# Kernel tuning notes

Hardware: AMD Instinct MI355X
Metric: run time of the kernel (lower is better)

The kernel has to match this reference:

```python
import jax, jax.numpy as jnp
import numpy as np

N = 4096      # sequence length (tokens)
D = 256       # model_dim
H = 4         # num_heads
DH = D // H   # dim_per_head = 64
TOPK = 30     # dot_attention default
SCALE = float((DH // H) ** -0.5)  # torch: (key.size(-1)//num_heads)**-0.5 = 16**-0.5 = 0.25
LN_EPS = 1e-5


def setup_inputs() -> dict:
    key = jax.random.key(0)
    ks = jax.random.split(key, 11)
    s = 0.02
    return {
        "key_in":   jax.random.normal(ks[0], (N, D), jnp.float32),
        "value_in": jax.random.normal(ks[1], (N, D), jnp.float32),
        "query_in": jax.random.normal(ks[2], (N, D), jnp.float32),
        "Wq": jax.random.normal(ks[3], (D, D), jnp.float32) * s,
        "bq": jax.random.normal(ks[4], (D,), jnp.float32) * s,
        "Wk": jax.random.normal(ks[5], (D, D), jnp.float32) * s,
        "bk": jax.random.normal(ks[6], (D,), jnp.float32) * s,
        "Wv": jax.random.normal(ks[7], (D, D), jnp.float32) * s,
        "bv": jax.random.normal(ks[8], (D,), jnp.float32) * s,
        "Wo": jax.random.normal(ks[9], (D, D), jnp.float32) * s,
        "bo": jax.random.normal(ks[10], (D,), jnp.float32) * s,
        "ln_g": jnp.ones((D,), jnp.float32),
        "ln_b": jnp.zeros((D,), jnp.float32),
    }


def reference(key_in, value_in, query_in, Wq, bq, Wk, bk, Wv, bv, Wo, bo, ln_g, ln_b):
    # Projections (nn.Linear: x @ W.T + b)
    q = query_in @ Wq.T + bq            # (N, D)
    k = key_in @ Wk.T + bk
    v = value_in @ Wv.T + bv
    # view(N, H, DH).transpose(0,1) -> (H, N, DH)
    qh = q.reshape(N, H, DH).transpose(1, 0, 2)
    kh = k.reshape(N, H, DH).transpose(1, 0, 2)
    vh = v.reshape(N, H, DH).transpose(1, 0, 2)

    scores = jnp.einsum('hnd,hmd->hnm', qh, kh) * SCALE   # (H, N, N)

    # top-k mask via scatter (faithful to torch.topk + scatter_)
    idx = jax.lax.top_k(scores, TOPK)[1]                  # (H, N, TOPK)
    mask = jnp.zeros_like(scores).at[
        jnp.arange(H)[:, None, None],
        jnp.arange(N)[None, :, None],
        idx].set(1.0)
    masked = jnp.where(mask > 0, scores, -jnp.inf)
    attn = jax.nn.softmax(masked, axis=-1)                # (H, N, N); dropout p=0 -> identity

    ctx = jnp.einsum('hnm,hmd->hnd', attn, vh)            # (H, N, DH)
    ctx = ctx.transpose(1, 0, 2).reshape(N, D)

    out = ctx @ Wo.T + bo
    resid = query_in + out                                # residual is pre-projection query
    mu = resid.mean(axis=-1, keepdims=True)
    var = resid.var(axis=-1, keepdims=True)               # biased var, like torch LayerNorm
    out = (resid - mu) / jnp.sqrt(var + LN_EPS) * ln_g + ln_b
    return out, attn
```

## Files before the change

### kernel.cpp

```cpp
#include <hip/hip_runtime.h>
#include <stdint.h>

#define N_TOK 4096
#define DIM   256
#define NH    4
#define DH    64
#define TOPK  30
#define CANDN 40
#define ATT_SCALE 0.25f
#define LN_EPS 1e-5f

typedef __attribute__((ext_vector_type(8))) short bf16x8;
typedef __attribute__((ext_vector_type(4))) float f32x4;

static __device__ __forceinline__ ushort f2bf(float f) {
    uint x = __float_as_uint(f);
    return (ushort)((x + 0x7FFFu + ((x >> 16) & 1u)) >> 16);
}
static __device__ __forceinline__ bf16x8 load_frag(const ushort* p) {
    union { int4 i; bf16x8 f; } u;
    u.i = *reinterpret_cast<const int4*>(p);
    return u.f;
}
static __device__ __forceinline__ uint s16key(uint u) {
    return (u & 0x8000u) ? (u ^ 0xFFFFu) : (u | 0x8000u);
}

#define BK 32
__global__ __launch_bounds__(256) void qk_gemm_f32(
    const float* __restrict__ query_in, const float* __restrict__ key_in,
    const float* __restrict__ Wq, const float* __restrict__ bq,
    const float* __restrict__ Wk, const float* __restrict__ bk,
    float* __restrict__ qf, float* __restrict__ kf,
    ushort* __restrict__ qb, ushort* __restrict__ kb)
{
    const int j0g = blockIdx.x * 64;
    const int sel = j0g >> 8;
    const int j0  = j0g & 255;
    const float* A    = sel ? key_in : query_in;
    const float* W    = sel ? Wk : Wq;
    const float* bias = sel ? bk : bq;
    float*  outF = sel ? kf : qf;
    ushort* outB = sel ? kb : qb;

    __shared__ float As[BK][64 + 4];
    __shared__ float Ws[BK][64 + 4];
    const int tid = threadIdx.x;
    const int tx = tid & 15;
    const int ty = tid >> 4;
    const int i0 = blockIdx.y * 64;

    float acc[4][4];
#pragma unroll
    for (int r = 0; r < 4; r++)
#pragma unroll
        for (int c = 0; c < 4; c++) acc[r][c] = 0.f;

    for (int k0 = 0; k0 < DIM; k0 += BK) {
#pragma unroll
        for (int u = 0; u < 2; u++) {
            const int f = u * 256 + tid;
            const int r = f >> 3;
            const int c = (f & 7) * 4;
            float4 va = *reinterpret_cast<const float4*>(A + (size_t)(i0 + r) * DIM + k0 + c);
            As[c + 0][r] = va.x; As[c + 1][r] = va.y;
            As[c + 2][r] = va.z; As[c + 3][r] = va.w;
            float4 vw = *reinterpret_cast<const float4*>(W + (size_t)(j0 + r) * DIM + k0 + c);
            Ws[c + 0][r] = vw.x; Ws[c + 1][r] = vw.y;
            Ws[c + 2][r] = vw.z; Ws[c + 3][r] = vw.w;
        }
        __syncthreads();
#pragma unroll
        for (int kk = 0; kk < BK; kk++) {
            const float4 a4 = *reinterpret_cast<const float4*>(&As[kk][ty * 4]);
            const float4 b4 = *reinterpret_cast<const float4*>(&Ws[kk][tx * 4]);
            const float ar[4] = {a4.x, a4.y, a4.z, a4.w};
            const float br[4] = {b4.x, b4.y, b4.z, b4.w};
#pragma unroll
            for (int r = 0; r < 4; r++)
#pragma unroll
                for (int c = 0; c < 4; c++) acc[r][c] += ar[r] * br[c];
        }
        __syncthreads();
    }

#pragma unroll
    for (int r = 0; r < 4; r++) {
        const int gi = i0 + ty * 4 + r;
#pragma unroll
        for (int c = 0; c < 4; c++) {
            const int gj = j0 + tx * 4 + c;
            float v = acc[r][c] + bias[gj];
            outF[(size_t)gi * DIM + gj] = v;
            outB[(size_t)gi * DIM + gj] = f2bf(v);
        }
    }
}

__global__ __launch_bounds__(256) void cast_kernel(
    const float* __restrict__ value_in, const float* __restrict__ Wv,
    const float* __restrict__ Wo, ushort* __restrict__ value_b,
    ushort* __restrict__ Wv_b, ushort* __restrict__ Wo_b)
{
    const int id4 = blockIdx.x * 256 + threadIdx.x;
    const int NV = 1048576 / 4, NW = 65536 / 4;
    const float* src; ushort* dst; int off;
    if (id4 < NV)            { src = value_in; dst = value_b; off = id4; }
    else if (id4 < NV + NW)  { src = Wv; dst = Wv_b; off = id4 - NV; }
    else                     { src = Wo; dst = Wo_b; off = id4 - NV - NW; }
    float4 v = reinterpret_cast<const float4*>(src)[off];
    ushort4 o = {f2bf(v.x), f2bf(v.y), f2bf(v.z), f2bf(v.w)};
    reinterpret_cast<ushort4*>(dst)[off] = o;
}

__global__ __launch_bounds__(256) void mfma_gemm(
    const ushort* __restrict__ A, const ushort* __restrict__ B,
    const float* __restrict__ bias, const float* __restrict__ addX,
    float* __restrict__ outF)
{
    const int lane = threadIdx.x & 63;
    const int wv   = threadIdx.x >> 6;
    const int i0   = blockIdx.y * 64 + wv * 16;
    const int j0   = blockIdx.x * 64;
    const int r = lane & 15, q = lane >> 4;

    f32x4 acc[4];
#pragma unroll
    for (int b = 0; b < 4; b++) acc[b] = (f32x4){0.f, 0.f, 0.f, 0.f};

#pragma unroll
    for (int ks = 0; ks < 8; ks++) {
        const int kk = ks * 32 + q * 8;
        bf16x8 af = load_frag(A + (size_t)(i0 + r) * DIM + kk);
        bf16x8 bfr[4];
#pragma unroll
        for (int jt = 0; jt < 4; jt++)
            bfr[jt] = load_frag(B + (size_t)(j0 + jt * 16 + r) * DIM + kk);
#pragma unroll
        for (int jt = 0; jt < 4; jt++)
            acc[jt] = __builtin_amdgcn_mfma_f32_16x16x32_bf16(af, bfr[jt], acc[jt], 0, 0, 0);
    }

#pragma unroll
    for (int jt = 0; jt < 4; jt++) {
        const int gj = j0 + jt * 16 + r;
        const float bv = bias[gj];
#pragma unroll
        for (int rg = 0; rg < 4; rg++) {
            const int gi = i0 + q * 4 + rg;
            float v = acc[jt][rg] + bv;
            if (addX) v += addX[(size_t)gi * DIM + gj];
            outF[(size_t)gi * DIM + gj] = v;
        }
    }
}

__global__ __launch_bounds__(256) void scores_kernel(
    const ushort* __restrict__ qb, const ushort* __restrict__ kb,
    ushort* __restrict__ sb)
{
    const int lane = threadIdx.x & 63;
    const int wv   = threadIdx.x >> 6;
    const int h    = blockIdx.z;
    const int i0   = blockIdx.y * 128 + wv * 32;
    const int j0   = blockIdx.x * 128;
    const int r = lane & 15, q = lane >> 4;
    const int koff = h * DH;

    f32x4 acc[2][8];
#pragma unroll
    for (int a = 0; a < 2; a++)
#pragma unroll
        for (int b = 0; b < 8; b++) acc[a][b] = (f32x4){0.f, 0.f, 0.f, 0.f};

#pragma unroll
    for (int ks = 0; ks < 2; ks++) {
        const int kk = koff + ks * 32 + q * 8;
        bf16x8 af[2], bfr[8];
#pragma unroll
        for (int mt = 0; mt < 2; mt++)
            af[mt] = load_frag(qb + (size_t)(i0 + mt * 16 + r) * DIM + kk);
#pragma unroll
        for (int jt = 0; jt < 8; jt++)
            bfr[jt] = load_frag(kb + (size_t)(j0 + jt * 16 + r) * DIM + kk);
#pragma unroll
        for (int mt = 0; mt < 2; mt++)
#pragma unroll
            for (int jt = 0; jt < 8; jt++)
                acc[mt][jt] = __builtin_amdgcn_mfma_f32_16x16x32_bf16(
                    af[mt], bfr[jt], acc[mt][jt], 0, 0, 0);
    }

#pragma unroll
    for (int mt = 0; mt < 2; mt++)
#pragma unroll
        for (int rg = 0; rg < 4; rg++) {
            const int gi = i0 + mt * 16 + q * 4 + rg;
            ushort* row = sb + ((size_t)(h * N_TOK + gi)) * N_TOK;
#pragma unroll
            for (int jt = 0; jt < 8; jt++)
                row[j0 + jt * 16 + r] = (ushort)s16key(f2bf(acc[mt][jt][rg]));
        }
}

__global__ __launch_bounds__(256) void select_kernel(
    const ushort* __restrict__ sb, const float* __restrict__ qf,
    const float* __restrict__ kf, const float* __restrict__ vf,
    float* __restrict__ pval, int* __restrict__ pidx,
    ushort* __restrict__ ctxb)
{
    const int lane = threadIdx.x & 63;
    const int wv   = threadIdx.x >> 6;
    const int row  = blockIdx.x * 4 + wv;
    const int h    = row >> 12;
    const int i    = row & (N_TOK - 1);
    const ushort* srow = sb + (size_t)row * N_TOK;

    __shared__ uint  hist[4][256];
    __shared__ uint  cand[4][64];
    __shared__ uint  ccnt[4];
    __shared__ float pw[4][TOPK];
    __shared__ int   jw[4][TOPK];
    __shared__ __align__(16) float qsh[4][DH];

    qsh[wv][lane] = qf[(size_t)i * DIM + h * DH + lane];
    if (lane == 0) ccnt[wv] = 0;
#pragma unroll
    for (int b = 0; b < 4; b++) hist[wv][b * 64 + lane] = 0u;

    uint kw[32];
    const int4* srow4 = reinterpret_cast<const int4*>(srow);
#pragma unroll
    for (int t = 0; t < 8; t++) {
        int4 c = srow4[t * 64 + lane];
        kw[t * 4 + 0] = (uint)c.x; kw[t * 4 + 1] = (uint)c.y;
        kw[t * 4 + 2] = (uint)c.z; kw[t * 4 + 3] = (uint)c.w;
    }

    uint mx = 0;
#pragma unroll
    for (int w = 0; w < 32; w++) {
        uint lo16 = kw[w] & 0xFFFFu, hi16 = kw[w] >> 16;
        mx = max(mx, max(lo16, hi16));
    }
#pragma unroll
    for (int off = 32; off; off >>= 1)
        mx = max(mx, (uint)__shfl_xor((int)mx, off));

    __syncthreads();

#pragma unroll
    for (int w = 0; w < 32; w++) {
        uint d0 = mx - (kw[w] & 0xFFFFu);
        uint d1 = mx - (kw[w] >> 16);
        if (d0 < 255u) atomicAdd(&hist[wv][d0], 1u);
        if (d1 < 255u) atomicAdd(&hist[wv][d1], 1u);
    }
    __syncthreads();

    const uint c0 = hist[wv][lane * 4 + 0];
    const uint c1 = hist[wv][lane * 4 + 1];
    const uint c2 = hist[wv][lane * 4 + 2];
    const uint c3 = hist[wv][lane * 4 + 3];
    const uint seg = c0 + c1 + c2 + c3;
    uint scan = seg;
#pragma unroll
    for (int d = 1; d < 64; d <<= 1) {
        uint y = (uint)__shfl_up((int)scan, d);
        if (lane >= d) scan += y;
    }
    const uint excl = scan - seg;
    const bool crossing = (excl < CANDN) && (scan >= CANDN);
    unsigned long long bal = __ballot(crossing);

    int t = 256;
    if (bal != 0ull) {
        const int srcLane = __ffsll(bal) - 1;
        int tloc = lane * 4;
        if (crossing) {
            uint cum = excl + c0;
            if (cum < CANDN) { tloc++; cum += c1;
                if (cum < CANDN) { tloc++; cum += c2;
                    if (cum < CANDN) { tloc++; } } }
        }
        t = __shfl(tloc, srcLane);
    }

    uint T;
    if (t <= 254) {
        T = mx - (uint)t;
    } else {
        uint lo = 0;
#pragma unroll
        for (int b = 15; b >= 0; b--) {
            uint trial = lo | (1u << b);
            int c = 0;
#pragma unroll
            for (int w = 0; w < 32; w++) {
                c += ((kw[w] & 0xFFFFu) >= trial) ? 1 : 0;
                c += ((kw[w] >> 16)     >= trial) ? 1 : 0;
            }
#pragma unroll
            for (int off = 32; off; off >>= 1) c += __shfl_xor(c, off);
            if (c >= CANDN) lo = trial;
        }
        T = lo;
    }

#pragma unroll
    for (int w = 0; w < 32; w++) {
        const uint lo16 = kw[w] & 0xFFFFu, hi16 = kw[w] >> 16;
        const int jbase = (w >> 2) * 512 + lane * 8 + (w & 3) * 2;
        if (lo16 >= T) {
            uint pos = atomicAdd(&ccnt[wv], 1u);
            if (pos < 64u) cand[wv][pos] = (uint)jbase;
        }
        if (hi16 >= T) {
            uint pos = atomicAdd(&ccnt[wv], 1u);
            if (pos < 64u) cand[wv][pos] = (uint)(jbase + 1);
        }
    }
    __syncthreads();
    const int m = (int)min(ccnt[wv], 64u);

    unsigned long long ukey = 0ull;
    if (lane < m) {
        const int j = (int)cand[wv][lane];
        const float4* kr = reinterpret_cast<const float4*>(kf + (size_t)j * DIM + h * DH);
        const float4* qr = reinterpret_cast<const float4*>(qsh[wv]);
        float s = 0.f;
#pragma unroll
        for (int d = 0; d < 16; d++) {
            float4 a = qr[d], bb = kr[d];
            s += a.x * bb.x; s += a.y * bb.y; s += a.z * bb.z; s += a.w * bb.w;
        }
        uint bits = __float_as_uint(s);
        uint s32 = (bits & 0x80000000u) ? ~bits : (bits | 0x80000000u);
        ukey = ((unsigned long long)s32 << 12) | (unsigned long long)(4095 - j);
    }

#pragma unroll
    for (int k = 2; k <= 64; k <<= 1) {
#pragma unroll
        for (int jj = k >> 1; jj > 0; jj >>= 1) {
            unsigned long long o = __shfl_xor(ukey, jj);
            bool keepMax = ((lane & jj) != 0) ^ ((lane & k) != 0);
            ukey = keepMax ? (ukey > o ? ukey : o) : (ukey < o ? ukey : o);
        }
    }

    const int rank = 63 - lane;
    const int jsel = 4095 - (int)(ukey & 0xFFFull);
    uint s32b = (uint)(ukey >> 12);
    uint fb = (s32b & 0x80000000u) ? (s32b ^ 0x80000000u) : ~s32b;
    const float sc = __uint_as_float(fb);
    const float stop = __shfl(sc, 63);

    float e = (rank < TOPK) ? __expf((sc - stop) * ATT_SCALE) : 0.f;
    float esum = e;
#pragma unroll
    for (int off = 32; off; off >>= 1) esum += __shfl_xor(esum, off);
    const float p = e / esum;

    if (rank < TOPK) {
        pw[wv][rank] = p; jw[wv][rank] = jsel;
        pval[(size_t)row * 32 + rank] = p;
        pidx[(size_t)row * 32 + rank] = jsel;
    }
    __syncthreads();

    float a = 0.f;
#pragma unroll
    for (int c = 0; c < TOPK; c++)
        a += pw[wv][c] * vf[(size_t)jw[wv][c] * DIM + h * DH + lane];
    ctxb[(size_t)i * DIM + h * DH + lane] = f2bf(a);
}

__global__ __launch_bounds__(256) void attn_write(
    const float* __restrict__ pval, const int* __restrict__ pidx,
    float* __restrict__ attnF)
{
    __shared__ __align__(16) float rb[4][N_TOK];
    const int tid = threadIdx.x;
    const int r0 = blockIdx.x * 4;

    float4* rb4 = reinterpret_cast<float4*>(&rb[0][0]);
    const float4 z = {0.f, 0.f, 0.f, 0.f};
#pragma unroll
    for (int t = 0; t < 16; t++) rb4[t * 256 + tid] = z;
    __syncthreads();
    if (tid < 4 * TOPK) {
        const int w = tid / TOPK, c = tid % TOPK;
        rb[w][pidx[(size_t)(r0 + w) * 32 + c]] = pval[(size_t)(r0 + w) * 32 + c];
    }
    __syncthreads();
#pragma unroll
    for (int w = 0; w < 4; w++) {
        float4* grow = reinterpret_cast<float4*>(attnF + (size_t)(r0 + w) * N_TOK);
#pragma unroll
        for (int t = 0; t < 4; t++)
            grow[t * 256 + tid] = rb4[w * 1024 + t * 256 + tid];
    }
}

__global__ __launch_bounds__(64) void ln_kernel(
    float* __restrict__ resb, const float* __restrict__ g,
    const float* __restrict__ b)
{
    const int i = blockIdx.x, lane = threadIdx.x;
    float4* rowp = reinterpret_cast<float4*>(resb + (size_t)i * DIM);
    float4 x = rowp[lane];
    float s  = x.x + x.y + x.z + x.w;
    float sq = x.x * x.x + x.y * x.y + x.z * x.z + x.w * x.w;
#pragma unroll
    for (int off = 32; off; off >>= 1) {
        s  += __shfl_xor(s, off);
        sq += __shfl_xor(sq, off);
    }
    const float mu  = s * (1.f / DIM);
    const float var = sq * (1.f / DIM) - mu * mu;
    const float rstd = rsqrtf(var + LN_EPS);
    const int col = lane * 4;
    float4 o;
    o.x = (x.x - mu) * rstd * g[col + 0] + b[col + 0];
    o.y = (x.y - mu) * rstd * g[col + 1] + b[col + 1];
    o.z = (x.z - mu) * rstd * g[col + 2] + b[col + 2];
    o.w = (x.w - mu) * rstd * g[col + 3] + b[col + 3];
    rowp[lane] = o;
}

extern "C" void kernel_launch(void* const* d_in, const int* in_sizes, int n_in,
                              void* d_out, int out_size, void* d_ws, size_t ws_size,
                              hipStream_t stream)
{
    const float* key_in   = (const float*)d_in[0];
    const float* value_in = (const float*)d_in[1];
    const float* query_in = (const float*)d_in[2];
    const float* Wq = (const float*)d_in[3];
    const float* bq = (const float*)d_in[4];
    const float* Wk = (const float*)d_in[5];
    const float* bk = (const float*)d_in[6];
    const float* Wv = (const float*)d_in[7];
    const float* bv = (const float*)d_in[8];
    const float* Wo = (const float*)d_in[9];
    const float* bo = (const float*)d_in[10];
    const float* ln_g = (const float*)d_in[11];
    const float* ln_b = (const float*)d_in[12];

    float* outF  = (float*)d_out;
    float* attnF = outF + (size_t)N_TOK * DIM;

    const size_t SC = 33554432;
    ushort* sb   = (ushort*)attnF;
    float*  qf   = attnF + SC;
    float*  kf   = attnF + SC + 1048576;
    float*  vf   = attnF + SC + 2097152;
    ushort* qb   = (ushort*)(attnF + SC + 3145728);
    ushort* kb   = (ushort*)(attnF + SC + 3670016);
    ushort* ctxb = (ushort*)(attnF + SC + 4194304);

    float*  pval    = (float*)d_ws;
    int*    pidx    = (int*)d_ws + 524288;
    ushort* value_b = (ushort*)((char*)d_ws + (4u << 20));
    ushort* Wv_b    = (ushort*)((char*)d_ws + (6u << 20));
    ushort* Wo_b    = (ushort*)((char*)d_ws + (6u << 20) + 131072);

    cast_kernel<<<dim3((1048576 + 65536 + 65536) / 4 / 256), 256, 0, stream>>>(
        value_in, Wv, Wo, value_b, Wv_b, Wo_b);
    qk_gemm_f32<<<dim3(8, 64), 256, 0, stream>>>(
        query_in, key_in, Wq, bq, Wk, bk, qf, kf, qb, kb);
    mfma_gemm<<<dim3(4, 64), 256, 0, stream>>>(value_b, Wv_b, bv, nullptr, vf);

    scores_kernel<<<dim3(32, 32, NH), 256, 0, stream>>>(qb, kb, sb);
    select_kernel<<<dim3(N_TOK * NH / 4), 256, 0, stream>>>(
        sb, qf, kf, vf, pval, pidx, ctxb);

    mfma_gemm<<<dim3(4, 64), 256, 0, stream>>>(ctxb, Wo_b, bo, query_in, outF);
    ln_kernel<<<N_TOK, 64, 0, stream>>>(outF, ln_g, ln_b);

    attn_write<<<N_TOK * NH / 4, 256, 0, stream>>>(pval, pidx, attnF);
}
```

Baseline: 440.5 us.

## Fuse attention-matrix write into select kernel and stage score stores via LDS

When the workspace is large enough, the score keys move into the workspace, so select_kernel can zero its attention row and scatter the top-k probabilities directly into the output. This drops the separate attn_write pass and the pval/pidx round-trip. The scores kernel now stages each wave's tile in shared memory and writes 16-byte coalesced rows instead of scattered 2-byte stores. Several block-wide barriers are removed because each wave only touches its own shared slices. Ordering between the zero-fill and the scatter relies on an explicit s_waitcnt, and the path needs a workspace of more than 128MB.

```diff
diff --git a/kernel.cpp b/kernel.cpp
--- a/kernel.cpp
+++ b/kernel.cpp
@@ -167,6 +167,8 @@
     const int r = lane & 15, q = lane >> 4;
     const int koff = h * DH;
 
+    __shared__ ushort st[4][32][136];
+
     f32x4 acc[2][8];
 #pragma unroll
     for (int a = 0; a < 2; a++)
@@ -194,20 +196,27 @@
 #pragma unroll
     for (int mt = 0; mt < 2; mt++)
 #pragma unroll
-        for (int rg = 0; rg < 4; rg++) {
-            const int gi = i0 + mt * 16 + q * 4 + rg;
-            ushort* row = sb + ((size_t)(h * N_TOK + gi)) * N_TOK;
-#pragma unroll
-            for (int jt = 0; jt < 8; jt++)
-                row[j0 + jt * 16 + r] = (ushort)s16key(f2bf(acc[mt][jt][rg]));
-        }
+        for (int jt = 0; jt < 8; jt++)
+#pragma unroll
+            for (int rg = 0; rg < 4; rg++)
+                st[wv][mt * 16 + q * 4 + rg][jt * 16 + r] =
+                    (ushort)s16key(f2bf(acc[mt][jt][rg]));
+
+    const int rr = lane >> 4, seg = lane & 15;
+#pragma unroll
+    for (int it = 0; it < 8; it++) {
+        const int rowl = it * 4 + rr;
+        const int gi = i0 + rowl;
+        int4 vdat = *reinterpret_cast<const int4*>(&st[wv][rowl][seg * 8]);
+        *reinterpret_cast<int4*>(sb + ((size_t)(h * N_TOK + gi)) * N_TOK + j0 + seg * 8) = vdat;
+    }
 }
 
 __global__ __launch_bounds__(256) void select_kernel(
     const ushort* __restrict__ sb, const float* __restrict__ qf,
     const float* __restrict__ kf, const float* __restrict__ vf,
     float* __restrict__ pval, int* __restrict__ pidx,
-    ushort* __restrict__ ctxb)
+    ushort* __restrict__ ctxb, float* __restrict__ attnRow)
 {
     const int lane = threadIdx.x & 63;
     const int wv   = threadIdx.x >> 6;
@@ -247,8 +256,6 @@
     for (int off = 32; off; off >>= 1)
         mx = max(mx, (uint)__shfl_xor((int)mx, off));
 
-    __syncthreads();
-
 #pragma unroll
     for (int w = 0; w < 32; w++) {
         uint d0 = mx - (kw[w] & 0xFFFFu);
@@ -256,7 +263,6 @@
         if (d0 < 255u) atomicAdd(&hist[wv][d0], 1u);
         if (d1 < 255u) atomicAdd(&hist[wv][d1], 1u);
     }
-    __syncthreads();
 
     const uint c0 = hist[wv][lane * 4 + 0];
     const uint c1 = hist[wv][lane * 4 + 1];
@@ -307,6 +313,13 @@
         T = lo;
     }
 
+    if (attnRow) {
+        float4* rowg = reinterpret_cast<float4*>(attnRow + (size_t)row * N_TOK);
+        const float4 z = {0.f, 0.f, 0.f, 0.f};
+#pragma unroll
+        for (int tt = 0; tt < 16; tt++) rowg[tt * 64 + lane] = z;
+    }
+
 #pragma unroll
     for (int w = 0; w < 32; w++) {
         const uint lo16 = kw[w] & 0xFFFFu, hi16 = kw[w] >> 16;
@@ -320,7 +333,6 @@
             if (pos < 64u) cand[wv][pos] = (uint)(jbase + 1);
         }
     }
-    __syncthreads();
     const int m = (int)min(ccnt[wv], 64u);
 
     unsigned long long ukey = 0ull;
@@ -364,16 +376,23 @@
 
     if (rank < TOPK) {
         pw[wv][rank] = p; jw[wv][rank] = jsel;
-        pval[(size_t)row * 32 + rank] = p;
-        pidx[(size_t)row * 32 + rank] = jsel;
-    }
-    __syncthreads();
+        if (pval) {
+            pval[(size_t)row * 32 + rank] = p;
+            pidx[(size_t)row * 32 + rank] = jsel;
+        }
+    }
 
     float a = 0.f;
 #pragma unroll
     for (int c = 0; c < TOPK; c++)
         a += pw[wv][c] * vf[(size_t)jw[wv][c] * DIM + h * DH + lane];
     ctxb[(size_t)i * DIM + h * DH + lane] = f2bf(a);
+
+    if (attnRow) {
+        asm volatile("s_waitcnt vmcnt(0)" ::: "memory");
+        if (rank < TOPK)
+            attnRow[(size_t)row * N_TOK + jsel] = p;
+    }
 }
 
 __global__ __launch_bounds__(256) void attn_write(
@@ -450,33 +469,63 @@
     float* outF  = (float*)d_out;
     float* attnF = outF + (size_t)N_TOK * DIM;
 
-    const size_t SC = 33554432;
-    ushort* sb   = (ushort*)attnF;
-    float*  qf   = attnF + SC;
-    float*  kf   = attnF + SC + 1048576;
-    float*  vf   = attnF + SC + 2097152;
-    ushort* qb   = (ushort*)(attnF + SC + 3145728);
-    ushort* kb   = (ushort*)(attnF + SC + 3670016);
-    ushort* ctxb = (ushort*)(attnF + SC + 4194304);
-
-    float*  pval    = (float*)d_ws;
-    int*    pidx    = (int*)d_ws + 524288;
-    ushort* value_b = (ushort*)((char*)d_ws + (4u << 20));
-    ushort* Wv_b    = (ushort*)((char*)d_ws + (6u << 20));
-    ushort* Wo_b    = (ushort*)((char*)d_ws + (6u << 20) + 131072);
-
-    cast_kernel<<<dim3((1048576 + 65536 + 65536) / 4 / 256), 256, 0, stream>>>(
-        value_in, Wv, Wo, value_b, Wv_b, Wo_b);
-    qk_gemm_f32<<<dim3(8, 64), 256, 0, stream>>>(
-        query_in, key_in, Wq, bq, Wk, bk, qf, kf, qb, kb);
-    mfma_gemm<<<dim3(4, 64), 256, 0, stream>>>(value_b, Wv_b, bv, nullptr, vf);
-
-    scores_kernel<<<dim3(32, 32, NH), 256, 0, stream>>>(qb, kb, sb);
-    select_kernel<<<dim3(N_TOK * NH / 4), 256, 0, stream>>>(
-        sb, qf, kf, vf, pval, pidx, ctxb);
-
-    mfma_gemm<<<dim3(4, 64), 256, 0, stream>>>(ctxb, Wo_b, bo, query_in, outF);
-    ln_kernel<<<N_TOK, 64, 0, stream>>>(outF, ln_g, ln_b);
-
-    attn_write<<<N_TOK * NH / 4, 256, 0, stream>>>(pval, pidx, attnF);
-}
+    const size_t KEYB = (size_t)NH * N_TOK * N_TOK * 2;
+    const size_t NEED = KEYB + (21u << 20);
+
+    if (ws_size >= NEED) {
+        char* ws = (char*)d_ws;
+        ushort* sb      = (ushort*)ws;
+        float*  qf      = (float*)(ws + KEYB);
+        float*  kf      = (float*)(ws + KEYB + (4u  << 20));
+        float*  vf      = (float*)(ws + KEYB + (8u  << 20));
+        ushort* qb      = (ushort*)(ws + KEYB + (12u << 20));
+        ushort* kb      = (ushort*)(ws + KEYB + (14u << 20));
+        ushort* ctxb    = (ushort*)(ws + KEYB + (16u << 20));
+        ushort* value_b = (ushort*)(ws + KEYB + (18u << 20));
+        ushort* Wv_b    = (ushort*)(ws + KEYB + (20u << 20));
+        ushort* Wo_b    = (ushort*)(ws + KEYB + (20u << 20) + 131072);
+
+        cast_kernel<<<dim3((1048576 + 65536 + 65536) / 4 / 256), 256, 0, stream>>>(
+            value_in, Wv, Wo, value_b, Wv_b, Wo_b);
+        qk_gemm_f32<<<dim3(8, 64), 256, 0, stream>>>(
+            query_in, key_in, Wq, bq, Wk, bk, qf, kf, qb, kb);
+        mfma_gemm<<<dim3(4, 64), 256, 0, stream>>>(value_b, Wv_b, bv, nullptr, vf);
+
+        scores_kernel<<<dim3(32, 32, NH), 256, 0, stream>>>(qb, kb, sb);
+        select_kernel<<<dim3(N_TOK * NH / 4), 256, 0, stream>>>(
+            sb, qf, kf, vf, nullptr, nullptr, ctxb, attnF);
+
+        mfma_gemm<<<dim3(4, 64), 256, 0, stream>>>(ctxb, Wo_b, bo, query_in, outF);
+        ln_kernel<<<N_TOK, 64, 0, stream>>>(outF, ln_g, ln_b);
+    } else {
+        const size_t SC = 33554432;
+        ushort* sb   = (ushort*)attnF;
+        float*  qf   = attnF + SC;
+        float*  kf   = attnF + SC + 1048576;
+        float*  vf   = attnF + SC + 2097152;
+        ushort* qb   = (ushort*)(attnF + SC + 3145728);
+        ushort* kb   = (ushort*)(attnF + SC + 3670016);
+        ushort* ctxb = (ushort*)(attnF + SC + 4194304);
+
+        float*  pval    = (float*)d_ws;
+        int*    pidx    = (int*)d_ws + 524288;
+        ushort* value_b = (ushort*)((char*)d_ws + (4u << 20));
+        ushort* Wv_b    = (ushort*)((char*)d_ws + (6u << 20));
+        ushort* Wo_b    = (ushort*)((char*)d_ws + (6u << 20) + 131072);
+
+        cast_kernel<<<dim3((1048576 + 65536 + 65536) / 4 / 256), 256, 0, stream>>>(
+            value_in, Wv, Wo, value_b, Wv_b, Wo_b);
+        qk_gemm_f32<<<dim3(8, 64), 256, 0, stream>>>(
+            query_in, key_in, Wq, bq, Wk, bk, qf, kf, qb, kb);
+        mfma_gemm<<<dim3(4, 64), 256, 0, stream>>>(value_b, Wv_b, bv, nullptr, vf);
+
+        scores_kernel<<<dim3(32, 32, NH), 256, 0, stream>>>(qb, kb, sb);
+        select_kernel<<<dim3(N_TOK * NH / 4), 256, 0, stream>>>(
+            sb, qf, kf, vf, pval, pidx, ctxb, nullptr);
+
+        mfma_gemm<<<dim3(4, 64), 256, 0, stream>>>(ctxb, Wo_b, bo, query_in, outF);
+        ln_kernel<<<N_TOK, 64, 0, stream>>>(outF, ln_g, ln_b);
+
+        attn_write<<<N_TOK * NH / 4, 256, 0, stream>>>(pval, pidx, attnF);
+    }
+}
```

After: 471.3 us. 1.07x slower.

## Store attention scores as 8-bit fixed-point keys for top-k candidate selection

Applied to the files above, without the earlier changes.

The scores kernel now quantises each score to an 8-bit key (floor(s*32)+128, clamped), stages it in shared memory and writes coalesced 16-byte rows. This halves the scratch score matrix traffic between the scores and select kernels. The select kernel builds a histogram with a fixed floor instead of a per-row max, gathers up to 192 candidates and ranks them in multiple bitonic rounds. A full fp32 recompute fallback handles rows with too many candidates. Intermediate buffers move into the workspace. The coarse quantisation risks more candidates per row and extra exact-dot work, plus fallback cost on outlier rows.

```diff
diff --git a/kernel.cpp b/kernel.cpp
--- a/kernel.cpp
+++ b/kernel.cpp
@@ -6,12 +6,15 @@
 #define NH    4
 #define DH    64
 #define TOPK  30
-#define CANDN 40
+#define CANDN 56
+#define CANDCAP 192
+#define FLOORK8 173u
 #define ATT_SCALE 0.25f
 #define LN_EPS 1e-5f
 
 typedef __attribute__((ext_vector_type(8))) short bf16x8;
 typedef __attribute__((ext_vector_type(4))) float f32x4;
+typedef unsigned long long u64;
 
 static __device__ __forceinline__ ushort f2bf(float f) {
     uint x = __float_as_uint(f);
@@ -25,6 +28,12 @@
 static __device__ __forceinline__ uint s16key(uint u) {
     return (u & 0x8000u) ? (u ^ 0xFFFFu) : (u | 0x8000u);
 }
+static __device__ __forceinline__ uint f2k8(float s) {
+    int v = (int)floorf(s * 32.0f) + 128;
+    return (uint)min(max(v, 0), 255);
+}
+static __device__ __forceinline__ u64 u64max(u64 a, u64 b) { return a > b ? a : b; }
+static __device__ __forceinline__ u64 u64min(u64 a, u64 b) { return a < b ? a : b; }
 
 #define BK 32
 __global__ __launch_bounds__(256) void qk_gemm_f32(
@@ -103,7 +112,7 @@
     ushort* __restrict__ Wv_b, ushort* __restrict__ Wo_b)
 {
     const int id4 = blockIdx.x * 256 + threadIdx.x;
-    const int NV = 1048576 / 4, NW = 65536 / 4;
+    const int NV = 262144, NW = 16384;
     const float* src; ushort* dst; int off;
     if (id4 < NV)            { src = value_in; dst = value_b; off = id4; }
     else if (id4 < NV + NW)  { src = Wv; dst = Wv_b; off = id4 - NV; }
@@ -157,7 +166,7 @@
 
 __global__ __launch_bounds__(256) void scores_kernel(
     const ushort* __restrict__ qb, const ushort* __restrict__ kb,
-    ushort* __restrict__ sb)
+    uchar* __restrict__ sb)
 {
     const int lane = threadIdx.x & 63;
     const int wv   = threadIdx.x >> 6;
@@ -167,6 +176,8 @@
     const int r = lane & 15, q = lane >> 4;
     const int koff = h * DH;
 
+    __shared__ uchar st[4][32][144];
+
     f32x4 acc[2][8];
 #pragma unroll
     for (int a = 0; a < 2; a++)
@@ -194,17 +205,24 @@
 #pragma unroll
     for (int mt = 0; mt < 2; mt++)
 #pragma unroll
-        for (int rg = 0; rg < 4; rg++) {
-            const int gi = i0 + mt * 16 + q * 4 + rg;
-            ushort* row = sb + ((size_t)(h * N_TOK + gi)) * N_TOK;
-#pragma unroll
-            for (int jt = 0; jt < 8; jt++)
-                row[j0 + jt * 16 + r] = (ushort)s16key(f2bf(acc[mt][jt][rg]));
-        }
+        for (int jt = 0; jt < 8; jt++)
+#pragma unroll
+            for (int rg = 0; rg < 4; rg++)
+                st[wv][mt * 16 + q * 4 + rg][jt * 16 + r] =
+                    (uchar)f2k8(acc[mt][jt][rg]);
+
+    const int rr = lane >> 3, seg = lane & 7;
+#pragma unroll
+    for (int it = 0; it < 4; it++) {
+        const int rowl = it * 8 + rr;
+        const int gi = i0 + rowl;
+        int4 vdat = *reinterpret_cast<const int4*>(&st[wv][rowl][seg * 16]);
+        *reinterpret_cast<int4*>(sb + ((size_t)(h * N_TOK + gi)) * N_TOK + j0 + seg * 16) = vdat;
+    }
 }
 
 __global__ __launch_bounds__(256) void select_kernel(
-    const ushort* __restrict__ sb, const float* __restrict__ qf,
+    const uchar* __restrict__ sb, const float* __restrict__ qf,
     const float* __restrict__ kf, const float* __restrict__ vf,
     float* __restrict__ pval, int* __restrict__ pidx,
     ushort* __restrict__ ctxb)
@@ -214,13 +232,13 @@
     const int row  = blockIdx.x * 4 + wv;
     const int h    = row >> 12;
     const int i    = row & (N_TOK - 1);
-    const ushort* srow = sb + (size_t)row * N_TOK;
-
-    __shared__ uint  hist[4][256];
-    __shared__ uint  cand[4][64];
-    __shared__ uint  ccnt[4];
-    __shared__ float pw[4][TOPK];
-    __shared__ int   jw[4][TOPK];
+    const uchar* srow = sb + (size_t)row * N_TOK;
+
+    __shared__ uint   hist[4][256];
+    __shared__ ushort cand[4][CANDCAP];
+    __shared__ uint   ccnt[4];
+    __shared__ float  pw[4][TOPK];
+    __shared__ int    jw[4][TOPK];
     __shared__ __align__(16) float qsh[4][DH];
 
     qsh[wv][lane] = qf[(size_t)i * DIM + h * DH + lane];
@@ -228,35 +246,24 @@
 #pragma unroll
     for (int b = 0; b < 4; b++) hist[wv][b * 64 + lane] = 0u;
 
-    uint kw[32];
+    uint kw[16];
     const int4* srow4 = reinterpret_cast<const int4*>(srow);
 #pragma unroll
-    for (int t = 0; t < 8; t++) {
+    for (int t = 0; t < 4; t++) {
         int4 c = srow4[t * 64 + lane];
         kw[t * 4 + 0] = (uint)c.x; kw[t * 4 + 1] = (uint)c.y;
         kw[t * 4 + 2] = (uint)c.z; kw[t * 4 + 3] = (uint)c.w;
     }
 
-    uint mx = 0;
-#pragma unroll
-    for (int w = 0; w < 32; w++) {
-        uint lo16 = kw[w] & 0xFFFFu, hi16 = kw[w] >> 16;
-        mx = max(mx, max(lo16, hi16));
-    }
-#pragma unroll
-    for (int off = 32; off; off >>= 1)
-        mx = max(mx, (uint)__shfl_xor((int)mx, off));
-
-    __syncthreads();
-
-#pragma unroll
-    for (int w = 0; w < 32; w++) {
-        uint d0 = mx - (kw[w] & 0xFFFFu);
-        uint d1 = mx - (kw[w] >> 16);
-        if (d0 < 255u) atomicAdd(&hist[wv][d0], 1u);
-        if (d1 < 255u) atomicAdd(&hist[wv][d1], 1u);
-    }
-    __syncthreads();
+#pragma unroll
+    for (int w = 0; w < 16; w++) {
+        const uint x = kw[w];
+#pragma unroll
+        for (int b = 0; b < 4; b++) {
+            const uint k8 = (x >> (8 * b)) & 255u;
+            if (k8 >= FLOORK8) atomicAdd(&hist[wv][255u - k8], 1u);
+        }
+    }
 
     const uint c0 = hist[wv][lane * 4 + 0];
     const uint c1 = hist[wv][lane * 4 + 1];
@@ -273,7 +280,7 @@
     const bool crossing = (excl < CANDN) && (scan >= CANDN);
     unsigned long long bal = __ballot(crossing);
 
-    int t = 256;
+    uint Tk;
     if (bal != 0ull) {
         const int srcLane = __ffsll(bal) - 1;
         int tloc = lane * 4;
@@ -283,13 +290,56 @@
                 if (cum < CANDN) { tloc++; cum += c2;
                     if (cum < CANDN) { tloc++; } } }
         }
-        t = __shfl(tloc, srcLane);
-    }
-
-    uint T;
-    if (t <= 254) {
-        T = mx - (uint)t;
+        const int t = __shfl(tloc, srcLane);
+        Tk = 255u - (uint)t;
     } else {
+        uint lo = 0;
+#pragma unroll
+        for (int b = 7; b >= 0; b--) {
+            uint trial = lo | (1u << b);
+            int c = 0;
+#pragma unroll
+            for (int w = 0; w < 16; w++)
+#pragma unroll
+                for (int bb = 0; bb < 4; bb++)
+                    c += (((kw[w] >> (8 * bb)) & 255u) >= trial) ? 1 : 0;
+#pragma unroll
+            for (int off = 32; off; off >>= 1) c += __shfl_xor(c, off);
+            if (c >= CANDN) lo = trial;
+        }
+        Tk = lo;
+    }
+
+#pragma unroll
+    for (int w = 0; w < 16; w++) {
+        const uint x = kw[w];
+        const int jbase = (w >> 2) * 1024 + lane * 16 + (w & 3) * 4;
+#pragma unroll
+        for (int b = 0; b < 4; b++) {
+            if (((x >> (8 * b)) & 255u) >= Tk) {
+                uint pos = atomicAdd(&ccnt[wv], 1u);
+                if (pos < CANDCAP) cand[wv][pos] = (ushort)(jbase + b);
+            }
+        }
+    }
+
+    uint cnt = ccnt[wv];
+    if (cnt > CANDCAP) {
+        uint kwf[32];
+        const float4* qr = reinterpret_cast<const float4*>(qsh[wv]);
+        for (int tt = 0; tt < 64; tt++) {
+            const int j = tt * 64 + lane;
+            const float4* kr = reinterpret_cast<const float4*>(kf + (size_t)j * DIM + h * DH);
+            float s = 0.f;
+#pragma unroll
+            for (int d = 0; d < 16; d++) {
+                float4 a = qr[d], bb = kr[d];
+                s += a.x * bb.x; s += a.y * bb.y; s += a.z * bb.z; s += a.w * bb.w;
+            }
+            const uint key = s16key(f2bf(s));
+            if (tt & 1) kwf[tt >> 1] |= key << 16;
+            else        kwf[tt >> 1] = key;
+        }
         uint lo = 0;
 #pragma unroll
         for (int b = 15; b >= 0; b--) {
@@ -297,61 +347,68 @@
             int c = 0;
 #pragma unroll
             for (int w = 0; w < 32; w++) {
-                c += ((kw[w] & 0xFFFFu) >= trial) ? 1 : 0;
-                c += ((kw[w] >> 16)     >= trial) ? 1 : 0;
+                c += ((kwf[w] & 0xFFFFu) >= trial) ? 1 : 0;
+                c += ((kwf[w] >> 16)     >= trial) ? 1 : 0;
             }
 #pragma unroll
             for (int off = 32; off; off >>= 1) c += __shfl_xor(c, off);
-            if (c >= CANDN) lo = trial;
-        }
-        T = lo;
-    }
-
-#pragma unroll
-    for (int w = 0; w < 32; w++) {
-        const uint lo16 = kw[w] & 0xFFFFu, hi16 = kw[w] >> 16;
-        const int jbase = (w >> 2) * 512 + lane * 8 + (w & 3) * 2;
-        if (lo16 >= T) {
-            uint pos = atomicAdd(&ccnt[wv], 1u);
-            if (pos < 64u) cand[wv][pos] = (uint)jbase;
-        }
-        if (hi16 >= T) {
-            uint pos = atomicAdd(&ccnt[wv], 1u);
-            if (pos < 64u) cand[wv][pos] = (uint)(jbase + 1);
-        }
-    }
-    __syncthreads();
-    const int m = (int)min(ccnt[wv], 64u);
-
-    unsigned long long ukey = 0ull;
-    if (lane < m) {
-        const int j = (int)cand[wv][lane];
-        const float4* kr = reinterpret_cast<const float4*>(kf + (size_t)j * DIM + h * DH);
-        const float4* qr = reinterpret_cast<const float4*>(qsh[wv]);
-        float s = 0.f;
-#pragma unroll
-        for (int d = 0; d < 16; d++) {
-            float4 a = qr[d], bb = kr[d];
-            s += a.x * bb.x; s += a.y * bb.y; s += a.z * bb.z; s += a.w * bb.w;
-        }
-        uint bits = __float_as_uint(s);
-        uint s32 = (bits & 0x80000000u) ? ~bits : (bits | 0x80000000u);
-        ukey = ((unsigned long long)s32 << 12) | (unsigned long long)(4095 - j);
-    }
-
-#pragma unroll
-    for (int k = 2; k <= 64; k <<= 1) {
-#pragma unroll
-        for (int jj = k >> 1; jj > 0; jj >>= 1) {
-            unsigned long long o = __shfl_xor(ukey, jj);
-            bool keepMax = ((lane & jj) != 0) ^ ((lane & k) != 0);
-            ukey = keepMax ? (ukey > o ? ukey : o) : (ukey < o ? ukey : o);
+            if (c >= 40) lo = trial;
+        }
+        if (lane == 0) ccnt[wv] = 0u;
+        for (int tt = 0; tt < 64; tt++) {
+            const uint key = (tt & 1) ? (kwf[tt >> 1] >> 16) : (kwf[tt >> 1] & 0xFFFFu);
+            if (key >= lo) {
+                uint pos = atomicAdd(&ccnt[wv], 1u);
+                if (pos < 64u) cand[wv][pos] = (ushort)(tt * 64 + lane);
+            }
+        }
+        cnt = min(ccnt[wv], 64u);
+    }
+
+    const int rounds = (int)((cnt + 63) >> 6);
+    u64 best = 0ull;
+    for (int rd = 0; rd < rounds; rd++) {
+        const int e = rd * 64 + lane;
+        u64 nk = 0ull;
+        if (e < (int)cnt) {
+            const int j = (int)cand[wv][e];
+            const float4* kr = reinterpret_cast<const float4*>(kf + (size_t)j * DIM + h * DH);
+            const float4* qr = reinterpret_cast<const float4*>(qsh[wv]);
+            float s = 0.f;
+#pragma unroll
+            for (int d = 0; d < 16; d++) {
+                float4 a = qr[d], bb = kr[d];
+                s += a.x * bb.x; s += a.y * bb.y; s += a.z * bb.z; s += a.w * bb.w;
+            }
+            uint bits = __float_as_uint(s);
+            uint s32 = (bits & 0x80000000u) ? ~bits : (bits | 0x80000000u);
+            nk = ((u64)s32 << 12) | (u64)(4095 - j);
+        }
+#pragma unroll
+        for (int k = 2; k <= 64; k <<= 1)
+#pragma unroll
+            for (int jj = k >> 1; jj > 0; jj >>= 1) {
+                u64 o = __shfl_xor(nk, jj);
+                bool keepMax = ((lane & jj) != 0) ^ ((lane & k) != 0);
+                nk = keepMax ? u64max(nk, o) : u64min(nk, o);
+            }
+        if (rd == 0) {
+            best = nk;
+        } else {
+            u64 rev = __shfl(nk, 63 - lane);
+            u64 m = u64max(best, rev);
+#pragma unroll
+            for (int jj = 32; jj; jj >>= 1) {
+                u64 o = __shfl_xor(m, jj);
+                m = ((lane & jj) != 0) ? u64max(m, o) : u64min(m, o);
+            }
+            best = m;
         }
     }
 
     const int rank = 63 - lane;
-    const int jsel = 4095 - (int)(ukey & 0xFFFull);
-    uint s32b = (uint)(ukey >> 12);
+    const int jsel = 4095 - (int)(best & 0xFFFull);
+    uint s32b = (uint)(best >> 12);
     uint fb = (s32b & 0x80000000u) ? (s32b ^ 0x80000000u) : ~s32b;
     const float sc = __uint_as_float(fb);
     const float stop = __shfl(sc, 63);
@@ -367,7 +424,6 @@
         pval[(size_t)row * 32 + rank] = p;
         pidx[(size_t)row * 32 + rank] = jsel;
     }
-    __syncthreads();
 
     float a = 0.f;
 #pragma unroll
@@ -450,22 +506,23 @@
     float* outF  = (float*)d_out;
     float* attnF = outF + (size_t)N_TOK * DIM;
 
-    const size_t SC = 33554432;
-    ushort* sb   = (ushort*)attnF;
-    float*  qf   = attnF + SC;
-    float*  kf   = attnF + SC + 1048576;
-    float*  vf   = attnF + SC + 2097152;
-    ushort* qb   = (ushort*)(attnF + SC + 3145728);
-    ushort* kb   = (ushort*)(attnF + SC + 3670016);
-    ushort* ctxb = (ushort*)(attnF + SC + 4194304);
-
-    float*  pval    = (float*)d_ws;
-    int*    pidx    = (int*)d_ws + 524288;
-    ushort* value_b = (ushort*)((char*)d_ws + (4u << 20));
-    ushort* Wv_b    = (ushort*)((char*)d_ws + (6u << 20));
-    ushort* Wo_b    = (ushort*)((char*)d_ws + (6u << 20) + 131072);
-
-    cast_kernel<<<dim3((1048576 + 65536 + 65536) / 4 / 256), 256, 0, stream>>>(
+    uchar* sb = (uchar*)attnF;
+
+    const size_t MB = 1u << 20;
+    char* ws = (char*)d_ws;
+    float*  qf      = (float*)(ws);
+    float*  kf      = (float*)(ws + 4 * MB);
+    float*  vf      = (float*)(ws + 8 * MB);
+    ushort* qb      = (ushort*)(ws + 12 * MB);
+    ushort* kb      = (ushort*)(ws + 14 * MB);
+    ushort* ctxb    = (ushort*)(ws + 16 * MB);
+    ushort* value_b = (ushort*)(ws + 18 * MB);
+    ushort* Wv_b    = (ushort*)(ws + 20 * MB);
+    ushort* Wo_b    = (ushort*)(ws + 20 * MB + 131072);
+    float*  pval    = (float*)(ws + 21 * MB);
+    int*    pidx    = (int*)(ws + 23 * MB);
+
+    cast_kernel<<<(262144 + 16384 + 16384) / 256, 256, 0, stream>>>(
         value_in, Wv, Wo, value_b, Wv_b, Wo_b);
     qk_gemm_f32<<<dim3(8, 64), 256, 0, stream>>>(
         query_in, key_in, Wq, bq, Wk, bk, qf, kf, qb, kb);
```

After: 486.7 us. +10.5%, slower.
